# Performance work log

Measured on AMD Instinct MI355X. Metric: run time of the kernel, lower is better.

The kernel has to match this reference:

```python
import jax, jax.numpy as jnp
import numpy as np

HEADS = 16
DIM_HEAD = 64
MAX_REL_POS = 16  # temporal_length


def setup_inputs() -> dict:
    key = jax.random.key(0)
    ks = jax.random.split(key, 8)
    B, T, D = 2048, 16, 1024
    inner = HEADS * DIM_HEAD  # 1024
    w = 0.02  # weight init scale for numerical stability
    return {
        "x": jax.random.normal(ks[0], (B, T, D), jnp.float32),
        "Wq": jax.random.normal(ks[1], (inner, D), jnp.float32) * w,
        "Wk": jax.random.normal(ks[2], (inner, D), jnp.float32) * w,
        "Wv": jax.random.normal(ks[3], (inner, D), jnp.float32) * w,
        "Wo": jax.random.normal(ks[4], (D, inner), jnp.float32) * w,
        "bo": jnp.zeros((D,), jnp.float32),
        "rel_k_table": jax.random.normal(ks[5], (2 * MAX_REL_POS + 1, DIM_HEAD), jnp.float32) * w,
        "rel_v_table": jax.random.normal(ks[6], (2 * MAX_REL_POS + 1, DIM_HEAD), jnp.float32) * w,
    }


def reference(x, Wq, Wk, Wv, Wo, bo, rel_k_table, rel_v_table):
    B, T, D = x.shape
    h, dh = HEADS, DIM_HEAD
    scale = dh ** -0.5

    def split_heads(t):  # [B,T,h*dh] -> [B*h,T,dh]
        return t.reshape(B, T, h, dh).transpose(0, 2, 1, 3).reshape(B * h, T, dh)

    q = split_heads(x @ Wq.T)
    k = split_heads(x @ Wk.T)
    v = split_heads(x @ Wv.T)

    sim = jnp.einsum('bid,bjd->bij', q, k) * scale

    # relative-position bias: idx[i,j] = clip(j-i, -L, L) + L
    r = jnp.arange(T)
    idx = jnp.clip(r[None, :] - r[:, None], -MAX_REL_POS, MAX_REL_POS) + MAX_REL_POS
    k2 = rel_k_table[idx]  # [T,T,dh]
    sim = sim + jnp.einsum('btd,tsd->bts', q, k2) * scale

    attn = jax.nn.softmax(sim, axis=-1)
    out = jnp.einsum('bij,bjd->bid', attn, v)
    v2 = rel_v_table[idx]  # [T,T,dh]
    out = out + jnp.einsum('bts,tsd->btd', attn, v2)

    out = out.reshape(B, h, T, dh).transpose(0, 2, 1, 3).reshape(B, T, h * dh)
    return out @ Wo.T + bo
```

## Files before the change

kernel.cpp:

```cpp
#include <hip/hip_runtime.h>

#define HEADS 16
#define DIM_HEAD 64
#define T_SEQ 16
#define D_MODEL 1024
#define MAX_REL 16

typedef _Float16 half8 __attribute__((ext_vector_type(8)));
typedef float f32x4 __attribute__((ext_vector_type(4)));

__global__ __launch_bounds__(256)
void cvt_f32_f16(const float* __restrict__ in, _Float16* __restrict__ out, int n8) {
  int i = blockIdx.x * blockDim.x + threadIdx.x;
  if (i >= n8) return;
  float4 a = ((const float4*)in)[2 * i];
  float4 b = ((const float4*)in)[2 * i + 1];
  half8 h;
  h[0] = (_Float16)a.x; h[1] = (_Float16)a.y;
  h[2] = (_Float16)a.z; h[3] = (_Float16)a.w;
  h[4] = (_Float16)b.x; h[5] = (_Float16)b.y;
  h[6] = (_Float16)b.z; h[7] = (_Float16)b.w;
  ((half8*)out)[i] = h;
}

__global__ __launch_bounds__(256)
void prep_tables(const float* __restrict__ relk, const float* __restrict__ relv,
                 _Float16* __restrict__ RKh, _Float16* __restrict__ RVth) {
  const int i = threadIdx.x;
  {
    int m = i >> 3, d0 = (i & 7) * 8;
    float4 a = *(const float4*)(relk + m * 64 + d0);
    float4 b = *(const float4*)(relk + m * 64 + d0 + 4);
    half8 h;
    h[0] = (_Float16)a.x; h[1] = (_Float16)a.y;
    h[2] = (_Float16)a.z; h[3] = (_Float16)a.w;
    h[4] = (_Float16)b.x; h[5] = (_Float16)b.y;
    h[6] = (_Float16)b.z; h[7] = (_Float16)b.w;
    *(half8*)(RKh + m * 64 + d0) = h;
  }
  {
    int d = i >> 2, m0 = (i & 3) * 8;
    half8 h;
#pragma unroll
    for (int e = 0; e < 8; ++e) h[e] = (_Float16)relv[(m0 + e) * 64 + d];
    *(half8*)(RVth + d * 32 + m0) = h;
  }
}

__device__ __forceinline__ void gload_lds16(const _Float16* g, _Float16* l) {
  __builtin_amdgcn_global_load_lds(
      (const __attribute__((address_space(1))) unsigned int*)(uintptr_t)g,
      (__attribute__((address_space(3))) unsigned int*)(uintptr_t)l, 16, 0, 0);
}

template <bool OUT_F16>
__global__ __launch_bounds__(512, 2)
void gemm256(const _Float16* __restrict__ A, const _Float16* __restrict__ B,
             const float* __restrict__ bias, void* __restrict__ Cv,
             int M, int N, int K) {
  __shared__ _Float16 lds[2][2][2][128][64];
  const int tid = threadIdx.x;
  const int wave = tid >> 6, lane = tid & 63;
  const int wm = wave >> 2, wn = wave & 3;

  const int GN = N >> 8;
  const int nwg = gridDim.x;
  const int q = nwg >> 3, r = nwg & 7;
  const int xcd = blockIdx.x & 7, pos = blockIdx.x >> 3;
  const int wgid = (xcd < r ? xcd * (q + 1) : r * (q + 1) + (xcd - r) * q) + pos;
  const int bm = wgid / GN, bn = wgid % GN;

  const int fr = lane & 15;
  const int q4 = lane >> 4;
  const int l3 = lane >> 3;
  const int sl = (lane & 7) ^ l3;

  const _Float16* Ag = A + (size_t)(bm * 256) * K;
  const _Float16* Bg = B + (size_t)(bn * 256) * K;

  f32x4 acc[8][4];
#pragma unroll
  for (int m = 0; m < 8; ++m)
#pragma unroll
    for (int n = 0; n < 4; ++n) acc[m][n] = (f32x4){0.f, 0.f, 0.f, 0.f};

  auto stage_group = [&](int buf, int ab, int g, const _Float16* G, int k0) {
    const _Float16* src = G + (size_t)(g * 8 + l3) * K + k0 + sl * 8;
    gload_lds16(src, &lds[buf][ab][g >> 4][(g & 15) * 8][0]);
  };
  auto lateg = [&](int idx) { return idx < 12 ? 4 + idx : 8 + idx; };

  auto ldA = [&](int buf, int mf, int ks) {
    unsigned off = (unsigned)((mf * 16 + fr) * 128 + (ks * 4 + q4) * 16) ^
                   (unsigned)((fr & 7) << 4);
    return *(const half8*)((const char*)&lds[buf][0][wm][0][0] + off);
  };
  auto ldB = [&](int buf, int nf, int ks) {
    int rowB = wn * 64 + nf * 16 + fr;
    unsigned off = (unsigned)((rowB & 127) * 128 + (ks * 4 + q4) * 16) ^
                   (unsigned)((fr & 7) << 4);
    return *(const half8*)((const char*)&lds[buf][1][rowB >> 7][0][0] + off);
  };

  half8 bF[4][2];
  auto mm = [&](int p, half8 (&af)[2][2]) {
    __builtin_amdgcn_s_setprio(1);
#pragma unroll
    for (int i = 0; i < 2; ++i)
#pragma unroll
      for (int nf = 0; nf < 4; ++nf)
#pragma unroll
        for (int ks = 0; ks < 2; ++ks)
          acc[p * 2 + i][nf] = __builtin_amdgcn_mfma_f32_16x16x32_f16(
              af[i][ks], bF[nf][ks], acc[p * 2 + i][nf], 0, 0, 0);
    __builtin_amdgcn_s_setprio(0);
  };

#pragma unroll
  for (int j = 0; j < 4; ++j) stage_group(0, 1, wave * 4 + j, Bg, 0);
  stage_group(0, 0, wave < 4 ? wave : wave + 12, Ag, 0);
#pragma unroll
  for (int j = 0; j < 3; ++j) stage_group(0, 0, lateg(3 * wave + j), Ag, 0);
  asm volatile("s_waitcnt vmcnt(0)" ::: "memory");
  __builtin_amdgcn_s_barrier();

  const int NT = K >> 6;
  for (int t = 0; t < NT; ++t) {
    const int cur = t & 1, nxt = cur ^ 1;
    const bool pf = (t + 1 < NT);
    const int k1 = (t + 1) << 6;
    half8 aF[2][2];

#pragma unroll
    for (int nf = 0; nf < 4; ++nf)
#pragma unroll
      for (int ks = 0; ks < 2; ++ks) bF[nf][ks] = ldB(cur, nf, ks);
#pragma unroll
    for (int i = 0; i < 2; ++i)
#pragma unroll
      for (int ks = 0; ks < 2; ++ks) aF[i][ks] = ldA(cur, i, ks);
    if (pf) {
      stage_group(nxt, 1, wave * 4 + 0, Bg, k1);
      stage_group(nxt, 1, wave * 4 + 1, Bg, k1);
    }
    asm volatile("s_waitcnt lgkmcnt(0)" ::: "memory");
    __builtin_amdgcn_sched_barrier(0);
    mm(0, aF);
    __builtin_amdgcn_sched_barrier(0);
    if (pf) asm volatile("s_waitcnt vmcnt(2)" ::: "memory");
    else    asm volatile("s_waitcnt vmcnt(0)" ::: "memory");
    __builtin_amdgcn_s_barrier();

#pragma unroll
    for (int i = 0; i < 2; ++i)
#pragma unroll
      for (int ks = 0; ks < 2; ++ks) aF[i][ks] = ldA(cur, 2 + i, ks);
    if (pf) {
      stage_group(nxt, 1, wave * 4 + 2, Bg, k1);
      stage_group(nxt, 1, wave * 4 + 3, Bg, k1);
    }
    asm volatile("s_waitcnt lgkmcnt(0)" ::: "memory");
    __builtin_amdgcn_sched_barrier(0);
    mm(1, aF);
    __builtin_amdgcn_sched_barrier(0);
    __builtin_amdgcn_s_barrier();

#pragma unroll
    for (int i = 0; i < 2; ++i)
#pragma unroll
      for (int ks = 0; ks < 2; ++ks) aF[i][ks] = ldA(cur, 4 + i, ks);
    if (pf) {
      stage_group(nxt, 0, wave < 4 ? wave : wave + 12, Ag, k1);
      stage_group(nxt, 0, lateg(3 * wave + 0), Ag, k1);
    }
    asm volatile("s_waitcnt lgkmcnt(0)" ::: "memory");
    __builtin_amdgcn_sched_barrier(0);
    mm(2, aF);
    __builtin_amdgcn_sched_barrier(0);
    __builtin_amdgcn_s_barrier();

#pragma unroll
    for (int i = 0; i < 2; ++i)
#pragma unroll
      for (int ks = 0; ks < 2; ++ks) aF[i][ks] = ldA(cur, 6 + i, ks);
    if (pf) {
      stage_group(nxt, 0, lateg(3 * wave + 1), Ag, k1);
      stage_group(nxt, 0, lateg(3 * wave + 2), Ag, k1);
    }
    asm volatile("s_waitcnt lgkmcnt(0)" ::: "memory");
    __builtin_amdgcn_sched_barrier(0);
    mm(3, aF);
    __builtin_amdgcn_sched_barrier(0);
    if (pf) asm volatile("s_waitcnt vmcnt(3)" ::: "memory");
    __builtin_amdgcn_s_barrier();
  }

  const int row_l = q4 * 4;
#pragma unroll
  for (int mf = 0; mf < 8; ++mf) {
#pragma unroll
    for (int nf = 0; nf < 4; ++nf) {
      int col = bn * 256 + wn * 64 + nf * 16 + fr;
#pragma unroll
      for (int r4 = 0; r4 < 4; ++r4) {
        int row = bm * 256 + wm * 128 + mf * 16 + row_l + r4;
        if (OUT_F16) {
          ((_Float16*)Cv)[(size_t)row * N + col] = (_Float16)acc[mf][nf][r4];
        } else {
          ((float*)Cv)[(size_t)row * N + col] = acc[mf][nf][r4] + bias[col];
        }
      }
    }
  }
}

__global__ __launch_bounds__(256)
void attn_mfma(const _Float16* __restrict__ QKV,
               const _Float16* __restrict__ RKh, const _Float16* __restrict__ RVth,
               _Float16* __restrict__ O) {
  __shared__ _Float16 PB[4][16][72];
  __shared__ _Float16 VtP[4][64][40];

  const int tid = threadIdx.x;
  const int wave = tid >> 6, lane = tid & 63;

#pragma unroll
  for (int z = 0; z < 6; ++z) {
    int idx = z * 64 + lane;
    int row = idx / 24, cd = idx % 24;
    *(unsigned int*)&PB[wave][row][16 + 2 * cd] = 0u;
  }
#pragma unroll
  for (int z = 0; z < 8; ++z) {
    int idx = z * 64 + lane;
    int row = idx >> 3, cd = idx & 7;
    *(unsigned int*)&VtP[wave][row][16 + 2 * cd] = 0u;
  }

  const int bh = blockIdx.x * 4 + wave;
  const int b = bh >> 4, h = bh & 15;
  const size_t qbase = (size_t)(b * T_SEQ) * 3072 + h * 64;
  const int fr = lane & 15, fk8 = (lane >> 4) * 8;

  half8 aQ0 = *(const half8*)(QKV + qbase + (size_t)fr * 3072 + fk8);
  half8 aQ1 = *(const half8*)(QKV + qbase + (size_t)fr * 3072 + 32 + fk8);
  half8 bK0 = *(const half8*)(QKV + qbase + 1024 + (size_t)fr * 3072 + fk8);
  half8 bK1 = *(const half8*)(QKV + qbase + 1024 + (size_t)fr * 3072 + 32 + fk8);

  half8 rk0a = *(const half8*)(RKh + fr * 64 + fk8);
  half8 rk0b = *(const half8*)(RKh + fr * 64 + 32 + fk8);
  half8 rk1a = *(const half8*)(RKh + (16 + fr) * 64 + fk8);
  half8 rk1b = *(const half8*)(RKh + (16 + fr) * 64 + 32 + fk8);

  {
    const _Float16* vp = QKV + qbase + 2048 + (size_t)fr * 3072 + (lane >> 4) * 16;
    half8 v0 = *(const half8*)vp;
    half8 v1 = *(const half8*)(vp + 8);
    int d0 = (lane >> 4) * 16;
#pragma unroll
    for (int e = 0; e < 8; ++e) VtP[wave][d0 + e][fr] = v0[e];
#pragma unroll
    for (int e = 0; e < 8; ++e) VtP[wave][d0 + 8 + e][fr] = v1[e];
  }

  f32x4 accS = {0.f, 0.f, 0.f, 0.f};
  accS = __builtin_amdgcn_mfma_f32_16x16x32_f16(aQ0, bK0, accS, 0, 0, 0);
  accS = __builtin_amdgcn_mfma_f32_16x16x32_f16(aQ1, bK1, accS, 0, 0, 0);

  f32x4 G0 = {0.f, 0.f, 0.f, 0.f}, G1 = {0.f, 0.f, 0.f, 0.f};
  G0 = __builtin_amdgcn_mfma_f32_16x16x32_f16(aQ0, rk0a, G0, 0, 0, 0);
  G0 = __builtin_amdgcn_mfma_f32_16x16x32_f16(aQ1, rk0b, G0, 0, 0, 0);
  G1 = __builtin_amdgcn_mfma_f32_16x16x32_f16(aQ0, rk1a, G1, 0, 0, 0);
  G1 = __builtin_amdgcn_mfma_f32_16x16x32_f16(aQ1, rk1b, G1, 0, 0, 0);

  const int ibase = (lane >> 4) * 4;
#pragma unroll
  for (int r = 0; r < 4; ++r) {
    const int i = ibase + r;
    const int ridx = fr - i + MAX_REL;
    const int src = (lane & 48) | (ridx & 15);
    float g0 = __shfl(G0[r], src);
    float g1 = __shfl(G1[r], src);
    float g = (ridx >= 16) ? g1 : g0;
    float s = (accS[r] + g) * 0.125f;
    float mx = s;
#pragma unroll
    for (int w = 8; w >= 1; w >>= 1) mx = fmaxf(mx, __shfl_xor(mx, w));
    float e = __expf(s - mx);
    float sum = e;
#pragma unroll
    for (int w = 8; w >= 1; w >>= 1) sum += __shfl_xor(sum, w);
    _Float16 ph = (_Float16)(e / sum);
    PB[wave][i][fr] = ph;
    PB[wave][i][32 + (fr - i + MAX_REL)] = ph;
  }

  half8 aP0 = *(const half8*)&PB[wave][fr][fk8];
  half8 aP1 = *(const half8*)&PB[wave][fr][32 + fk8];
  const size_t obase = (size_t)(b * T_SEQ) * D_MODEL + h * 64;
#pragma unroll
  for (int t = 0; t < 4; ++t) {
    half8 bv = *(const half8*)&VtP[wave][t * 16 + fr][fk8];
    half8 br = *(const half8*)(RVth + (t * 16 + fr) * 32 + fk8);
    f32x4 o = {0.f, 0.f, 0.f, 0.f};
    o = __builtin_amdgcn_mfma_f32_16x16x32_f16(aP0, bv, o, 0, 0, 0);
    o = __builtin_amdgcn_mfma_f32_16x16x32_f16(aP1, br, o, 0, 0, 0);
#pragma unroll
    for (int r = 0; r < 4; ++r)
      O[obase + (size_t)(ibase + r) * D_MODEL + t * 16 + fr] = (_Float16)o[r];
  }
}

extern "C" void kernel_launch(void* const* d_in, const int* in_sizes, int n_in,
                              void* d_out, int out_size, void* d_ws, size_t ws_size,
                              hipStream_t stream) {
  const float* x  = (const float*)d_in[0];
  const float* Wq = (const float*)d_in[1];
  const float* Wk = (const float*)d_in[2];
  const float* Wv = (const float*)d_in[3];
  const float* Wo = (const float*)d_in[4];
  const float* bo = (const float*)d_in[5];
  const float* rk = (const float*)d_in[6];
  const float* rv = (const float*)d_in[7];
  float* out = (float*)d_out;

  const int total_rows = 2048 * T_SEQ;
  const size_t wsz = (size_t)D_MODEL * D_MODEL;

  _Float16* Wqkvh = (_Float16*)d_ws;
  _Float16* Woh  = Wqkvh + 3 * wsz;
  _Float16* RKh  = Woh + wsz;
  _Float16* RVth = RKh + 2048;
  _Float16* chunk_base = RVth + 2048;

  {
    int n8 = (int)(wsz / 8);
    int blocks = (n8 + 255) / 256;
    cvt_f32_f16<<<blocks, 256, 0, stream>>>(Wq, Wqkvh, n8);
    cvt_f32_f16<<<blocks, 256, 0, stream>>>(Wk, Wqkvh + wsz, n8);
    cvt_f32_f16<<<blocks, 256, 0, stream>>>(Wv, Wqkvh + 2 * wsz, n8);
    cvt_f32_f16<<<blocks, 256, 0, stream>>>(Wo, Woh, n8);
    prep_tables<<<1, 256, 0, stream>>>(rk, rv, RKh, RVth);
  }

  const size_t per_row_bytes = (size_t)5120 * sizeof(_Float16);
  size_t avail = ws_size - (size_t)(4 * wsz + 4096) * sizeof(_Float16);
  size_t rows_fit = avail / per_row_bytes;
  int rows_c = (rows_fit > (size_t)total_rows) ? total_rows : (int)rows_fit;
  rows_c = (rows_c / 256) * 256;
  if (rows_c < 256) rows_c = 256;

  for (int r0 = 0; r0 < total_rows; r0 += rows_c) {
    int rc = total_rows - r0;
    if (rc > rows_c) rc = rows_c;

    _Float16* xh   = chunk_base;
    _Float16* QKVb = xh + (size_t)rows_c * 1024;
    _Float16* AO   = QKVb + (size_t)rows_c * 3072;

    {
      int n8 = rc * 128;
      cvt_f32_f16<<<(n8 + 255) / 256, 256, 0, stream>>>(
          x + (size_t)r0 * D_MODEL, xh, n8);
    }

    gemm256<true><<<(3072 / 256) * (rc / 256), 512, 0, stream>>>(
        xh, Wqkvh, nullptr, QKVb, rc, 3072, 1024);

    attn_mfma<<<rc / 4, 256, 0, stream>>>(QKVb, RKh, RVth, AO);

    gemm256<false><<<(1024 / 256) * (rc / 256), 512, 0, stream>>>(
        AO, Woh, bo, out + (size_t)r0 * D_MODEL, rc, 1024, 1024);
  }
}
```

Baseline: 416.1 us.

## Fuse fp32-to-fp16 conversion of x into QKV GEMM A-operand staging

Drops the separate cvt kernel for x. The QKV GEMM now reads fp32 rows of x into registers one K-tile ahead, converts them to fp16 and writes them into LDS with the same swizzle layout. B staging is also reordered into half-tiles, and the per-iteration vmcnt waits are changed to a full drain at the end of each iteration. This removes one fp16 write and read of the whole activation tensor plus a launch, at the cost of doubled A global traffic in fp32, more registers and a less overlapped prefetch schedule.

```diff
diff --git a/kernel.cpp b/kernel.cpp
--- a/kernel.cpp
+++ b/kernel.cpp
@@ -53,9 +53,9 @@
       (__attribute__((address_space(3))) unsigned int*)(uintptr_t)l, 16, 0, 0);
 }
 
-template <bool OUT_F16>
+template <bool OUT_F16, bool A_F32>
 __global__ __launch_bounds__(512, 2)
-void gemm256(const _Float16* __restrict__ A, const _Float16* __restrict__ B,
+void gemm256(const void* __restrict__ Av, const _Float16* __restrict__ B,
              const float* __restrict__ bias, void* __restrict__ Cv,
              int M, int N, int K) {
   __shared__ _Float16 lds[2][2][2][128][64];
@@ -75,7 +75,8 @@
   const int l3 = lane >> 3;
   const int sl = (lane & 7) ^ l3;
 
-  const _Float16* Ag = A + (size_t)(bm * 256) * K;
+  const _Float16* Ag16 = (const _Float16*)Av + (size_t)(bm * 256) * K;
+  const float*    Ag32 = (const float*)Av + (size_t)(bm * 256) * K;
   const _Float16* Bg = B + (size_t)(bn * 256) * K;
 
   f32x4 acc[8][4];
@@ -84,11 +85,40 @@
 #pragma unroll
     for (int n = 0; n < 4; ++n) acc[m][n] = (f32x4){0.f, 0.f, 0.f, 0.f};
 
-  auto stage_group = [&](int buf, int ab, int g, const _Float16* G, int k0) {
-    const _Float16* src = G + (size_t)(g * 8 + l3) * K + k0 + sl * 8;
-    gload_lds16(src, &lds[buf][ab][g >> 4][(g & 15) * 8][0]);
-  };
-  auto lateg = [&](int idx) { return idx < 12 ? 4 + idx : 8 + idx; };
+  auto stage_half = [&](int buf, int ab, int half, const _Float16* G, int k0) {
+#pragma unroll
+    for (int i = 0; i < 2; ++i) {
+      int g = wave * 2 + i;
+      const _Float16* src =
+          G + (size_t)(half * 128 + g * 8 + l3) * K + k0 + sl * 8;
+      gload_lds16(src, &lds[buf][ab][half][g * 8][0]);
+    }
+  };
+
+  f32x4 pend[2][2][2];
+  auto ldA32 = [&](f32x4 (&dst)[2][2][2], int k0) {
+#pragma unroll
+    for (int h = 0; h < 2; ++h)
+#pragma unroll
+      for (int i = 0; i < 2; ++i) {
+        const float* s =
+            Ag32 + (size_t)(h * 128 + (wave * 2 + i) * 8 + l3) * K + k0 + sl * 8;
+        dst[h][i][0] = *(const f32x4*)s;
+        dst[h][i][1] = *(const f32x4*)(s + 4);
+      }
+  };
+  auto writeAhalf = [&](int buf, int h, f32x4 (&src)[2][2][2]) {
+#pragma unroll
+    for (int i = 0; i < 2; ++i) {
+      half8 v;
+#pragma unroll
+      for (int e = 0; e < 4; ++e) {
+        v[e] = (_Float16)src[h][i][0][e];
+        v[4 + e] = (_Float16)src[h][i][1][e];
+      }
+      *(half8*)((char*)&lds[buf][0][h][(wave * 2 + i) * 8][0] + lane * 16) = v;
+    }
+  };
 
   auto ldA = [&](int buf, int mf, int ks) {
     unsigned off = (unsigned)((mf * 16 + fr) * 128 + (ks * 4 + q4) * 16) ^
@@ -116,18 +146,35 @@
     __builtin_amdgcn_s_setprio(0);
   };
 
-#pragma unroll
-  for (int j = 0; j < 4; ++j) stage_group(0, 1, wave * 4 + j, Bg, 0);
-  stage_group(0, 0, wave < 4 ? wave : wave + 12, Ag, 0);
-#pragma unroll
-  for (int j = 0; j < 3; ++j) stage_group(0, 0, lateg(3 * wave + j), Ag, 0);
-  asm volatile("s_waitcnt vmcnt(0)" ::: "memory");
+  const int NT = K >> 6;
+
+  if constexpr (A_F32) {
+    f32x4 t0[2][2][2];
+    ldA32(t0, 0);
+    stage_half(0, 1, 0, Bg, 0);
+    stage_half(0, 1, 1, Bg, 0);
+    writeAhalf(0, 0, t0);
+    writeAhalf(0, 1, t0);
+    if (NT > 1) {
+      ldA32(pend, 64);
+      asm volatile("s_waitcnt vmcnt(4)" ::: "memory");
+    } else {
+      asm volatile("s_waitcnt vmcnt(0)" ::: "memory");
+    }
+    asm volatile("s_waitcnt lgkmcnt(0)" ::: "memory");
+  } else {
+    stage_half(0, 0, 0, Ag16, 0);
+    stage_half(0, 0, 1, Ag16, 0);
+    stage_half(0, 1, 0, Bg, 0);
+    stage_half(0, 1, 1, Bg, 0);
+    asm volatile("s_waitcnt vmcnt(0)" ::: "memory");
+  }
   __builtin_amdgcn_s_barrier();
 
-  const int NT = K >> 6;
   for (int t = 0; t < NT; ++t) {
     const int cur = t & 1, nxt = cur ^ 1;
     const bool pf = (t + 1 < NT);
+    const bool pf2 = (t + 2 < NT);
     const int k1 = (t + 1) << 6;
     half8 aF[2][2];
 
@@ -140,15 +187,13 @@
 #pragma unroll
       for (int ks = 0; ks < 2; ++ks) aF[i][ks] = ldA(cur, i, ks);
     if (pf) {
-      stage_group(nxt, 1, wave * 4 + 0, Bg, k1);
-      stage_group(nxt, 1, wave * 4 + 1, Bg, k1);
+      if constexpr (A_F32) writeAhalf(nxt, 0, pend);
+      else stage_half(nxt, 0, 0, Ag16, k1);
     }
     asm volatile("s_waitcnt lgkmcnt(0)" ::: "memory");
     __builtin_amdgcn_sched_barrier(0);
     mm(0, aF);
     __builtin_amdgcn_sched_barrier(0);
-    if (pf) asm volatile("s_waitcnt vmcnt(2)" ::: "memory");
-    else    asm volatile("s_waitcnt vmcnt(0)" ::: "memory");
     __builtin_amdgcn_s_barrier();
 
 #pragma unroll
@@ -156,8 +201,12 @@
 #pragma unroll
       for (int ks = 0; ks < 2; ++ks) aF[i][ks] = ldA(cur, 2 + i, ks);
     if (pf) {
-      stage_group(nxt, 1, wave * 4 + 2, Bg, k1);
-      stage_group(nxt, 1, wave * 4 + 3, Bg, k1);
+      if constexpr (A_F32) {
+        writeAhalf(nxt, 1, pend);
+        if (pf2) ldA32(pend, (t + 2) << 6);
+      } else {
+        stage_half(nxt, 0, 1, Ag16, k1);
+      }
     }
     asm volatile("s_waitcnt lgkmcnt(0)" ::: "memory");
     __builtin_amdgcn_sched_barrier(0);
@@ -169,10 +218,7 @@
     for (int i = 0; i < 2; ++i)
 #pragma unroll
       for (int ks = 0; ks < 2; ++ks) aF[i][ks] = ldA(cur, 4 + i, ks);
-    if (pf) {
-      stage_group(nxt, 0, wave < 4 ? wave : wave + 12, Ag, k1);
-      stage_group(nxt, 0, lateg(3 * wave + 0), Ag, k1);
-    }
+    if (pf) stage_half(nxt, 1, 0, Bg, k1);
     asm volatile("s_waitcnt lgkmcnt(0)" ::: "memory");
     __builtin_amdgcn_sched_barrier(0);
     mm(2, aF);
@@ -183,15 +229,12 @@
     for (int i = 0; i < 2; ++i)
 #pragma unroll
       for (int ks = 0; ks < 2; ++ks) aF[i][ks] = ldA(cur, 6 + i, ks);
-    if (pf) {
-      stage_group(nxt, 0, lateg(3 * wave + 1), Ag, k1);
-      stage_group(nxt, 0, lateg(3 * wave + 2), Ag, k1);
-    }
+    if (pf) stage_half(nxt, 1, 1, Bg, k1);
     asm volatile("s_waitcnt lgkmcnt(0)" ::: "memory");
     __builtin_amdgcn_sched_barrier(0);
     mm(3, aF);
     __builtin_amdgcn_sched_barrier(0);
-    if (pf) asm volatile("s_waitcnt vmcnt(3)" ::: "memory");
+    if (pf) asm volatile("s_waitcnt vmcnt(0)" ::: "memory");
     __builtin_amdgcn_s_barrier();
   }
 
@@ -343,7 +386,7 @@
     prep_tables<<<1, 256, 0, stream>>>(rk, rv, RKh, RVth);
   }
 
-  const size_t per_row_bytes = (size_t)5120 * sizeof(_Float16);
+  const size_t per_row_bytes = (size_t)4096 * sizeof(_Float16);
   size_t avail = ws_size - (size_t)(4 * wsz + 4096) * sizeof(_Float16);
   size_t rows_fit = avail / per_row_bytes;
   int rows_c = (rows_fit > (size_t)total_rows) ? total_rows : (int)rows_fit;
@@ -354,22 +397,15 @@
     int rc = total_rows - r0;
     if (rc > rows_c) rc = rows_c;
 
-    _Float16* xh   = chunk_base;
-    _Float16* QKVb = xh + (size_t)rows_c * 1024;
+    _Float16* QKVb = chunk_base;
     _Float16* AO   = QKVb + (size_t)rows_c * 3072;
 
-    {
-      int n8 = rc * 128;
-      cvt_f32_f16<<<(n8 + 255) / 256, 256, 0, stream>>>(
-          x + (size_t)r0 * D_MODEL, xh, n8);
-    }
-
-    gemm256<true><<<(3072 / 256) * (rc / 256), 512, 0, stream>>>(
-        xh, Wqkvh, nullptr, QKVb, rc, 3072, 1024);
+    gemm256<true, true><<<(3072 / 256) * (rc / 256), 512, 0, stream>>>(
+        x + (size_t)r0 * D_MODEL, Wqkvh, nullptr, QKVb, rc, 3072, 1024);
 
     attn_mfma<<<rc / 4, 256, 0, stream>>>(QKVb, RKh, RVth, AO);
 
-    gemm256<false><<<(1024 / 256) * (rc / 256), 512, 0, stream>>>(
+    gemm256<false, false><<<(1024 / 256) * (rc / 256), 512, 0, stream>>>(
         AO, Woh, bo, out + (size_t)r0 * D_MODEL, rc, 1024, 1024);
   }
 }
```

New measurement: 499.8 us. 1.2x slower.
